# Kernel tuning notes

Hardware: AMD Instinct MI355X
Metric: run time of the kernel (lower is better)

Reference implementation:

```python
import jax, jax.numpy as jnp
import numpy as np

B, R, Z, H = 2048, 512, 256, 512
T = 16           # num_steps
NL = 3           # num_layers
SCALE = 0.05     # param init scale


def setup_inputs() -> dict:
    key = jax.random.key(0)
    ks = jax.random.split(key, 8)
    return {
        "r": jax.random.normal(ks[0], (B, R), jnp.float32),
        "noise0": jax.random.normal(ks[1], (B, Z), jnp.float32),
        "noise": jax.random.normal(ks[2], (T, B, Z), jnp.float32),
        "W0": jax.random.normal(ks[3], (Z + R, H), jnp.float32) * SCALE,
        "b0": jnp.zeros((H,), jnp.float32),
        "Wh": jax.random.normal(ks[4], (H, H), jnp.float32) * SCALE,
        "bh": jnp.zeros((H,), jnp.float32),
        "Wo": jax.random.normal(ks[5], (H, Z), jnp.float32) * SCALE,
        "bo": jnp.zeros((Z,), jnp.float32),
        "Wt": jax.random.normal(ks[6], (1, Z + R), jnp.float32) * SCALE,
        "bt": jnp.zeros((Z + R,), jnp.float32),
    }


def reference(r, noise0, noise, W0, b0, Wh, bh, Wo, bo, Wt, bt):
    dt = jnp.float32(1.0 / T)
    sqrt_dt = jnp.sqrt(dt)

    def score_fn(z, t_scaled):
        # time_embedding: Linear(1, z+r) then non-linearity, added to [z, r]
        temb = jax.nn.relu(t_scaled * Wt[0] + bt)            # (Z+R,)
        h = jnp.concatenate([z, r], axis=-1) + temb          # (B, Z+R)
        h = h @ W0 + b0                                      # (B, H)
        # faithful to buggy nn.Sequential: act x (NL-1), then the SAME
        # shared Linear(h,h) applied (NL-1) times
        for _ in range(NL - 1):
            h = jax.nn.relu(h)
        for _ in range(NL - 1):
            h = h @ Wh + bh
        return h @ Wo + bo                                   # (B, Z)

    def step(z_prev, xs):
        t, eps = xs
        # Euler-Maruyama forward step: mu = z + score * dt, sigma = sqrt(dt)
        z_mu = z_prev + score_fn(z_prev, t * dt) * dt
        z_sigma = sqrt_dt * jnp.ones_like(z_mu)
        z = z_mu + z_sigma * eps                             # reparameterize
        return z, (z, z_mu, z_sigma)

    ts = jnp.arange(1, T + 1, dtype=jnp.float32)
    # z_0 ~ N(0, get_sigma(0)=1)
    z0 = noise0
    _, (zs, mus, sigmas) = jax.lax.scan(step, z0, (ts, noise))
    zs = jnp.concatenate([z0[None], zs], axis=0)             # (T+1, B, Z)
    mus = jnp.concatenate([jnp.zeros((1, B, Z), zs.dtype), mus], axis=0)
    sigmas = jnp.concatenate([jnp.ones((1, B, Z), zs.dtype), sigmas], axis=0)
    return jnp.stack([zs, mus, sigmas])                      # (3, T+1, B, Z)
```

## Files before the change

kernel.cpp:

```cpp
#include <hip/hip_runtime.h>


typedef __bf16 bf16_t;
typedef bf16_t bf16x8 __attribute__((ext_vector_type(8)));
typedef float f32x4 __attribute__((ext_vector_type(4)));

#define MFMA16(a, b, c) __builtin_amdgcn_mfma_f32_16x16x32_bf16((a), (b), (c), 0, 0, 0)

__device__ __forceinline__ void glds16(const void* gsrc, void* ldst) {
  __builtin_amdgcn_global_load_lds(
      (const __attribute__((address_space(1))) unsigned int*)gsrc,
      (__attribute__((address_space(3))) unsigned int*)ldst, 16, 0, 0);
}

__device__ __forceinline__ void pack_body(const float* __restrict__ src, bf16_t* __restrict__ dst,
                                          int K, int N, int tid0) {
  int NT = N >> 4;
  if (tid0 >= (K >> 5) * NT * 64) return;
  int l = tid0 & 63, grp = tid0 >> 6;
  int nt = grp % NT, kt = grp / NT;
  int rr = l & 15, gg = l >> 4;
  const float* s = src + (size_t)(kt * 32 + 8 * gg) * N + nt * 16 + rr;
  bf16_t* d = dst + (size_t)tid0 * 8;
#pragma unroll
  for (int j = 0; j < 8; ++j) d[j] = (bf16_t)s[(size_t)j * N];
}

__global__ __launch_bounds__(256) void p1_kernel(
    const float* __restrict__ r, const float* __restrict__ noise0,
    const float* __restrict__ W0, const float* __restrict__ Wh,
    const float* __restrict__ Wo, const float* __restrict__ Wt, const float* __restrict__ bt,
    bf16_t* __restrict__ r_bf, bf16_t* __restrict__ Wh_bf,
    bf16_t* __restrict__ W0zp, bf16_t* __restrict__ W0rp, bf16_t* __restrict__ Wop,
    float* __restrict__ tadd, float* __restrict__ out)
{
  const int SLAB = 2048 * 256;
  const int SZ = 17 * SLAB;
  int bid = blockIdx.x, tid = threadIdx.x;
  if (bid < 9728) {
    int i = (bid * 256 + tid) * 4;
    if (i >= 19 * SLAB) return;
    float4 v; int dst;
    if (i < 17 * SLAB) { float x = (i < SLAB) ? 1.0f : 0.25f; v = make_float4(x, x, x, x); dst = 2 * SZ + i; }
    else if (i < 18 * SLAB) { v = make_float4(0.f, 0.f, 0.f, 0.f); dst = SZ + (i - 17 * SLAB); }
    else { v = *(const float4*)(noise0 + (i - 18 * SLAB)); dst = i - 18 * SLAB; }
    *(float4*)(out + dst) = v;
  } else if (bid < 10752) {
    int i = ((bid - 9728) * 256 + tid) * 4;
#pragma unroll
    for (int j = 0; j < 4; ++j) r_bf[i + j] = (bf16_t)r[i + j];
  } else if (bid < 11008) {
    int i = ((bid - 10752) * 256 + tid) * 4;
#pragma unroll
    for (int j = 0; j < 4; ++j) Wh_bf[i + j] = (bf16_t)Wh[i + j];
  } else if (bid < 11072) {
    pack_body(W0, W0zp, 256, 512, (bid - 11008) * 256 + tid);
  } else if (bid < 11200) {
    pack_body(W0 + 256 * 512, W0rp, 512, 512, (bid - 11072) * 256 + tid);
  } else if (bid < 11264) {
    pack_body(Wo, Wop, 512, 256, (bid - 11200) * 256 + tid);
  } else {
    int rel = bid - 11264;
    int t = rel >> 1, n = (rel & 1) * 256 + tid;
    float ts = (t + 1) * 0.0625f;
    float s = 0.f;
#pragma unroll 4
    for (int k = 0; k < 768; ++k) {
      float e = fmaxf(ts * Wt[k] + bt[k], 0.f);
      s = fmaf(e, W0[(size_t)k * 512 + n], s);
    }
    tadd[t * 512 + n] = s;
  }
}

__device__ __forceinline__ void gemm_dev(
    const bf16_t* __restrict__ A, const bf16_t* __restrict__ Bp, const float* __restrict__ bias,
    float* __restrict__ C, bf16_t* __restrict__ Cp,
    int N, int K, int rt, int ct, bool useBias, bool writeRM, bool writePacked)
{
  int tid = threadIdx.x;
  int l = tid & 63, w = tid >> 6;
  int rr = l & 15, gg = l >> 4;
  int rowbase = rt * 64 + w * 16, colbase = ct * 64;
  int NT = N >> 4;
  const bf16x8* Bv = (const bf16x8*)Bp;
  f32x4 acc[4] = {};
  for (int kt = 0; kt < (K >> 5); ++kt) {
    bf16x8 af = *(const bf16x8*)(A + (size_t)(rowbase + rr) * K + kt * 32 + 8 * gg);
#pragma unroll
    for (int nt = 0; nt < 4; ++nt) {
      bf16x8 bf = Bv[(size_t)(kt * NT + (colbase >> 4) + nt) * 64 + l];
      acc[nt] = MFMA16(af, bf, acc[nt]);
    }
  }
#pragma unroll
  for (int nt = 0; nt < 4; ++nt) {
    int col = colbase + nt * 16 + rr;
    float bv = useBias ? bias[col] : 0.f;
#pragma unroll
    for (int q = 0; q < 4; ++q) {
      int row = rowbase + 4 * gg + q;
      float vv = acc[nt][q] + bv;
      if (writeRM) C[(size_t)row * N + col] = vv;
      if (writePacked) {
        int ktr = row >> 5;
        int lane2 = (2 * (w & 1) + (gg >> 1)) * 16 + rr;
        int jj = 4 * (gg & 1) + q;
        Cp[(size_t)((ktr * NT + (colbase >> 4) + nt) * 64 + lane2) * 8 + jj] = (bf16_t)vv;
      }
    }
  }
}

__global__ __launch_bounds__(256) void p2_kernel(
    const bf16_t* __restrict__ r_bf, const bf16_t* __restrict__ W0rp, const float* __restrict__ b0,
    float* __restrict__ baseb,
    const bf16_t* __restrict__ Wh_bf, const bf16_t* __restrict__ Wop,
    float* __restrict__ T3f, bf16_t* __restrict__ T3p)
{
  int bid = blockIdx.x;
  if (bid < 256) gemm_dev(r_bf, W0rp, b0, baseb, nullptr, 512, 512, bid & 31, bid >> 5, true, true, false);
  else           gemm_dev(Wh_bf, Wop, nullptr, T3f, T3p, 256, 512, (bid - 256) & 7, (bid - 256) >> 3, false, true, true);
}

__global__ __launch_bounds__(256) void p3_kernel(
    const bf16_t* __restrict__ Wh_bf, const bf16_t* __restrict__ T3p, bf16_t* __restrict__ Wfp,
    const float* __restrict__ bh, const float* __restrict__ T3f, const float* __restrict__ Wo,
    const float* __restrict__ bo, float* __restrict__ bo2)
{
  int bid = blockIdx.x;
  if (bid < 32) {
    gemm_dev(Wh_bf, T3p, nullptr, nullptr, Wfp, 256, 512, bid & 7, bid >> 3, false, false, true);
  } else {
    int n = threadIdx.x;
    float s = bo[n];
#pragma unroll 4
    for (int k = 0; k < 512; ++k)
      s = fmaf(bh[k], T3f[k * 256 + n] + Wo[k * 256 + n], s);
    bo2[n] = s;
  }
}

__global__ __launch_bounds__(512) void diffusion_main_kernel(
    const bf16_t* __restrict__ wpack,
    const float* __restrict__ base,
    const float* __restrict__ tadd,
    const float* __restrict__ bo2,
    const float* __restrict__ noise0,
    const float* __restrict__ noise,
    float* __restrict__ out)
{
  __shared__ bf16_t zbuf[16 * 256];
  __shared__ bf16_t abuf[16 * 512];
  __shared__ char wbuf[2][65536];
  const int tid = threadIdx.x;
  const int w = tid >> 6, l = tid & 63;
  const int rr = l & 15, gg = l >> 4;
  const int brow = blockIdx.x << 4;
  const char* wdata = (const char*)wpack;

  f32x4 base_reg[4];
#pragma unroll
  for (int nt = 0; nt < 4; ++nt)
#pragma unroll
    for (int q = 0; q < 4; ++q)
      base_reg[nt][q] = base[(size_t)(brow + 4 * gg + q) * 512 + w * 64 + nt * 16 + rr];
  float bo_reg[2];
#pragma unroll
  for (int nt = 0; nt < 2; ++nt) bo_reg[nt] = bo2[w * 32 + nt * 16 + rr];

  f32x4 zst[2];
#pragma unroll
  for (int nt = 0; nt < 2; ++nt)
#pragma unroll
    for (int q = 0; q < 4; ++q)
      zst[nt][q] = noise0[(size_t)(brow + 4 * gg + q) * 256 + w * 32 + nt * 16 + rr];
#pragma unroll
  for (int nt = 0; nt < 2; ++nt)
#pragma unroll
    for (int q = 0; q < 4; ++q) {
      int row = 4 * gg + q, col = w * 32 + nt * 16 + rr;
      zbuf[(row * 256 + col) ^ ((row & 7) << 3)] = (bf16_t)zst[nt][q];
    }

  {
    const char* src = wdata;
    char* dstl = &wbuf[0][0];
#pragma unroll
    for (int it = 0; it < 8; ++it)
      glds16(src + it * 8192 + w * 1024 + l * 16, dstl + it * 8192 + w * 1024);
  }

  f32x4 acc1[4];
  f32x4 acc2[2];
  bf16x8 zf[8];
  float ep[2][4];
  float tv[4];

#pragma unroll 1
  for (int cc = 0; cc < 128; ++cc) {
    __syncthreads();
    if (cc + 1 < 128) {
      const char* src = wdata + (size_t)((cc + 1) & 7) * 65536;
      char* dstl = &wbuf[(cc + 1) & 1][0];
#pragma unroll
      for (int it = 0; it < 8; ++it)
        glds16(src + it * 8192 + w * 1024 + l * 16, dstl + it * 8192 + w * 1024);
    }
    const char* wb = &wbuf[cc & 1][0];
    const int ph = cc & 7;
    const int t = cc >> 3;

    if (ph < 4) {
      if (ph == 0) {
#pragma unroll
        for (int nt = 0; nt < 2; ++nt)
#pragma unroll
          for (int q = 0; q < 4; ++q)
            ep[nt][q] = noise[((size_t)t * 2048 + brow + 4 * gg + q) * 256 + w * 32 + nt * 16 + rr];
#pragma unroll
        for (int nt = 0; nt < 4; ++nt) tv[nt] = tadd[t * 512 + w * 64 + nt * 16 + rr];
#pragma unroll
        for (int kt = 0; kt < 8; ++kt) {
          int e = (rr * 256 + kt * 32 + 8 * gg) ^ ((rr & 7) << 3);
          zf[kt] = *(const bf16x8*)&zbuf[e];
        }
#pragma unroll
        for (int nt = 0; nt < 4; ++nt)
#pragma unroll
          for (int q = 0; q < 4; ++q) acc1[nt][q] = base_reg[nt][q] + tv[nt];
      }
#pragma unroll
      for (int ktl = 0; ktl < 2; ++ktl) {
        int fbase = ktl * 32 + w * 4;
#pragma unroll
        for (int nt = 0; nt < 4; ++nt) {
          bf16x8 wfrag = *(const bf16x8*)(wb + ((size_t)(fbase + nt) * 64 + l) * 16);
          acc1[nt] = MFMA16(zf[2 * ph + ktl], wfrag, acc1[nt]);
        }
      }
      if (ph == 3) {
#pragma unroll
        for (int nt = 0; nt < 4; ++nt)
#pragma unroll
          for (int q = 0; q < 4; ++q) {
            int row = 4 * gg + q, col = w * 64 + nt * 16 + rr;
            abuf[(row * 512 + col) ^ ((row & 7) << 3)] = (bf16_t)fmaxf(acc1[nt][q], 0.f);
          }
      }
    } else {
      if (ph == 4) {
#pragma unroll
        for (int nt = 0; nt < 2; ++nt)
#pragma unroll
          for (int q = 0; q < 4; ++q) acc2[nt][q] = bo_reg[nt];
      }
      const int pc = ph - 4;
#pragma unroll
      for (int ktl = 0; ktl < 4; ++ktl) {
        int ktg = pc * 4 + ktl;
        int e = (rr * 512 + ktg * 32 + 8 * gg) ^ ((rr & 7) << 3);
        bf16x8 afr = *(const bf16x8*)&abuf[e];
        int fbase = ktl * 16 + w * 2;
#pragma unroll
        for (int nt = 0; nt < 2; ++nt) {
          bf16x8 wfrag = *(const bf16x8*)(wb + ((size_t)(fbase + nt) * 64 + l) * 16);
          acc2[nt] = MFMA16(afr, wfrag, acc2[nt]);
        }
      }
      if (ph == 7) {
#pragma unroll
        for (int nt = 0; nt < 2; ++nt)
#pragma unroll
          for (int q = 0; q < 4; ++q) {
            int row = 4 * gg + q, col = w * 32 + nt * 16 + rr;
            int grow = brow + row;
            float mu = fmaf(acc2[nt][q], 0.0625f, zst[nt][q]);
            float zn = fmaf(ep[nt][q], 0.25f, mu);
            zst[nt][q] = zn;
            out[((size_t)(t + 1) * 2048 + grow) * 256 + col] = zn;
            out[((size_t)(17 + t + 1) * 2048 + grow) * 256 + col] = mu;
            zbuf[(row * 256 + col) ^ ((row & 7) << 3)] = (bf16_t)zn;
          }
      }
    }
  }
}

extern "C" void kernel_launch(void* const* d_in, const int* in_sizes, int n_in,
                              void* d_out, int out_size, void* d_ws, size_t ws_size,
                              hipStream_t stream) {
  const float* r   = (const float*)d_in[0];
  const float* n0  = (const float*)d_in[1];
  const float* nz  = (const float*)d_in[2];
  const float* W0  = (const float*)d_in[3];
  const float* b0  = (const float*)d_in[4];
  const float* Wh  = (const float*)d_in[5];
  const float* bh  = (const float*)d_in[6];
  const float* Wo  = (const float*)d_in[7];
  const float* bo  = (const float*)d_in[8];
  const float* Wt  = (const float*)d_in[9];
  const float* bt  = (const float*)d_in[10];
  float* out = (float*)d_out;

  char* ws = (char*)d_ws;
  size_t off = 0;
  auto alloc = [&](size_t bytes) -> char* {
    char* p = ws + off;
    off += (bytes + 255) & ~(size_t)255;
    return p;
  };
  bf16_t* r_bf  = (bf16_t*)alloc((size_t)2048 * 512 * 2);
  bf16_t* Wh_bf = (bf16_t*)alloc((size_t)512 * 512 * 2);
  bf16_t* wpack = (bf16_t*)alloc((size_t)512 * 1024);
  bf16_t* W0zp  = wpack;
  bf16_t* Wfp   = wpack + 131072;
  bf16_t* W0rp  = (bf16_t*)alloc((size_t)512 * 512 * 2);
  bf16_t* Wop   = (bf16_t*)alloc((size_t)512 * 256 * 2);
  float*  T3f   = (float*) alloc((size_t)512 * 256 * 4);
  bf16_t* T3p   = (bf16_t*)alloc((size_t)512 * 256 * 2);
  float*  baseb = (float*) alloc((size_t)2048 * 512 * 4);
  float*  taddb = (float*) alloc((size_t)16 * 512 * 4);
  float*  bo2b  = (float*) alloc((size_t)256 * 4);
  if (off > ws_size) return;

  p1_kernel<<<11296, 256, 0, stream>>>(r, n0, W0, Wh, Wo, Wt, bt,
                                       r_bf, Wh_bf, W0zp, W0rp, Wop, taddb, out);
  p2_kernel<<<288, 256, 0, stream>>>(r_bf, W0rp, b0, baseb, Wh_bf, Wop, T3f, T3p);
  p3_kernel<<<33, 256, 0, stream>>>(Wh_bf, T3p, Wfp, bh, T3f, Wo, bo, bo2b);
  diffusion_main_kernel<<<128, 512, 0, stream>>>(wpack, baseb, taddb, bo2b, n0, nz, out);
}
```

Baseline: 423.1 us.

## Keep fused weight in registers and stream W0z fragments directly from global

Drops the double-buffered 128KB LDS weight staging fed by global_load_lds. The fused Wh·Wo weight slice for each wave now sits permanently in registers (32 bf16x8 fragments), and W0z fragments are loaded straight from global/L2 on every timestep. The loop runs once per timestep with two barriers instead of 128 chunk iterations with a barrier each. This removes LDS traffic and per-chunk synchronisation, but raises register pressure (launch_bounds 512,2) and puts global load latency on the path of the first GEMM.

Result: slower. 475.9 us (+12.5%).

```diff
diff --git a/kernel.cpp b/kernel.cpp
--- a/kernel.cpp
+++ b/kernel.cpp
@@ -6,12 +6,6 @@
 typedef float f32x4 __attribute__((ext_vector_type(4)));
 
 #define MFMA16(a, b, c) __builtin_amdgcn_mfma_f32_16x16x32_bf16((a), (b), (c), 0, 0, 0)
-
-__device__ __forceinline__ void glds16(const void* gsrc, void* ldst) {
-  __builtin_amdgcn_global_load_lds(
-      (const __attribute__((address_space(1))) unsigned int*)gsrc,
-      (__attribute__((address_space(3))) unsigned int*)ldst, 16, 0, 0);
-}
 
 __device__ __forceinline__ void pack_body(const float* __restrict__ src, bf16_t* __restrict__ dst,
                                           int K, int N, int tid0) {
@@ -141,8 +135,9 @@
   }
 }
 
-__global__ __launch_bounds__(512) void diffusion_main_kernel(
-    const bf16_t* __restrict__ wpack,
+__global__ __launch_bounds__(512, 2) void diffusion_main_kernel(
+    const bf16_t* __restrict__ W0zp,
+    const bf16_t* __restrict__ Wfp,
     const float* __restrict__ base,
     const float* __restrict__ tadd,
     const float* __restrict__ bo2,
@@ -152,12 +147,22 @@
 {
   __shared__ bf16_t zbuf[16 * 256];
   __shared__ bf16_t abuf[16 * 512];
-  __shared__ char wbuf[2][65536];
   const int tid = threadIdx.x;
   const int w = tid >> 6, l = tid & 63;
   const int rr = l & 15, gg = l >> 4;
   const int brow = blockIdx.x << 4;
-  const char* wdata = (const char*)wpack;
+  const size_t SLAB = 2048 * 256;
+  const size_t SZ = 17 * SLAB;
+
+  const bf16x8* W0v = (const bf16x8*)W0zp;
+  const bf16x8* Wfv = (const bf16x8*)Wfp;
+
+  bf16x8 wfres[16][2];
+#pragma unroll
+  for (int kt = 0; kt < 16; ++kt)
+#pragma unroll
+    for (int nt = 0; nt < 2; ++nt)
+      wfres[kt][nt] = Wfv[(size_t)(kt * 16 + w * 2 + nt) * 64 + l];
 
   f32x4 base_reg[4];
 #pragma unroll
@@ -182,108 +187,83 @@
       int row = 4 * gg + q, col = w * 32 + nt * 16 + rr;
       zbuf[(row * 256 + col) ^ ((row & 7) << 3)] = (bf16_t)zst[nt][q];
     }
-
-  {
-    const char* src = wdata;
-    char* dstl = &wbuf[0][0];
-#pragma unroll
-    for (int it = 0; it < 8; ++it)
-      glds16(src + it * 8192 + w * 1024 + l * 16, dstl + it * 8192 + w * 1024);
-  }
-
-  f32x4 acc1[4];
-  f32x4 acc2[2];
-  bf16x8 zf[8];
-  float ep[2][4];
-  float tv[4];
+  __syncthreads();
 
 #pragma unroll 1
-  for (int cc = 0; cc < 128; ++cc) {
+  for (int t = 0; t < 16; ++t) {
+    float ep[2][4];
+#pragma unroll
+    for (int nt = 0; nt < 2; ++nt)
+#pragma unroll
+      for (int q = 0; q < 4; ++q)
+        ep[nt][q] = noise[((size_t)t * 2048 + brow + 4 * gg + q) * 256 + w * 32 + nt * 16 + rr];
+
+    f32x4 acc1[4];
+#pragma unroll
+    for (int nt = 0; nt < 4; ++nt) {
+      float tv = tadd[t * 512 + w * 64 + nt * 16 + rr];
+#pragma unroll
+      for (int q = 0; q < 4; ++q) acc1[nt][q] = base_reg[nt][q] + tv;
+    }
+
+#pragma unroll
+    for (int c = 0; c < 4; ++c) {
+      bf16x8 wst[2][4];
+#pragma unroll
+      for (int ktl = 0; ktl < 2; ++ktl)
+#pragma unroll
+        for (int nt = 0; nt < 4; ++nt)
+          wst[ktl][nt] = W0v[(size_t)((2 * c + ktl) * 32 + w * 4 + nt) * 64 + l];
+      bf16x8 zc[2];
+#pragma unroll
+      for (int ktl = 0; ktl < 2; ++ktl) {
+        int e = (rr * 256 + (2 * c + ktl) * 32 + 8 * gg) ^ ((rr & 7) << 3);
+        zc[ktl] = *(const bf16x8*)&zbuf[e];
+      }
+#pragma unroll
+      for (int ktl = 0; ktl < 2; ++ktl)
+#pragma unroll
+        for (int nt = 0; nt < 4; ++nt)
+          acc1[nt] = MFMA16(zc[ktl], wst[ktl][nt], acc1[nt]);
+    }
+
+#pragma unroll
+    for (int nt = 0; nt < 4; ++nt)
+#pragma unroll
+      for (int q = 0; q < 4; ++q) {
+        int row = 4 * gg + q, col = w * 64 + nt * 16 + rr;
+        abuf[(row * 512 + col) ^ ((row & 7) << 3)] = (bf16_t)fmaxf(acc1[nt][q], 0.f);
+      }
     __syncthreads();
-    if (cc + 1 < 128) {
-      const char* src = wdata + (size_t)((cc + 1) & 7) * 65536;
-      char* dstl = &wbuf[(cc + 1) & 1][0];
-#pragma unroll
-      for (int it = 0; it < 8; ++it)
-        glds16(src + it * 8192 + w * 1024 + l * 16, dstl + it * 8192 + w * 1024);
-    }
-    const char* wb = &wbuf[cc & 1][0];
-    const int ph = cc & 7;
-    const int t = cc >> 3;
-
-    if (ph < 4) {
-      if (ph == 0) {
-#pragma unroll
-        for (int nt = 0; nt < 2; ++nt)
-#pragma unroll
-          for (int q = 0; q < 4; ++q)
-            ep[nt][q] = noise[((size_t)t * 2048 + brow + 4 * gg + q) * 256 + w * 32 + nt * 16 + rr];
-#pragma unroll
-        for (int nt = 0; nt < 4; ++nt) tv[nt] = tadd[t * 512 + w * 64 + nt * 16 + rr];
-#pragma unroll
-        for (int kt = 0; kt < 8; ++kt) {
-          int e = (rr * 256 + kt * 32 + 8 * gg) ^ ((rr & 7) << 3);
-          zf[kt] = *(const bf16x8*)&zbuf[e];
-        }
-#pragma unroll
-        for (int nt = 0; nt < 4; ++nt)
-#pragma unroll
-          for (int q = 0; q < 4; ++q) acc1[nt][q] = base_reg[nt][q] + tv[nt];
+
+    f32x4 acc2[2];
+#pragma unroll
+    for (int nt = 0; nt < 2; ++nt)
+#pragma unroll
+      for (int q = 0; q < 4; ++q) acc2[nt][q] = bo_reg[nt];
+#pragma unroll
+    for (int kt = 0; kt < 16; ++kt) {
+      int e = (rr * 512 + kt * 32 + 8 * gg) ^ ((rr & 7) << 3);
+      bf16x8 af = *(const bf16x8*)&abuf[e];
+#pragma unroll
+      for (int nt = 0; nt < 2; ++nt)
+        acc2[nt] = MFMA16(af, wfres[kt][nt], acc2[nt]);
+    }
+
+#pragma unroll
+    for (int nt = 0; nt < 2; ++nt)
+#pragma unroll
+      for (int q = 0; q < 4; ++q) {
+        int row = 4 * gg + q, col = w * 32 + nt * 16 + rr;
+        int grow = brow + row;
+        float mu = fmaf(acc2[nt][q], 0.0625f, zst[nt][q]);
+        float zn = fmaf(ep[nt][q], 0.25f, mu);
+        zst[nt][q] = zn;
+        out[((size_t)(t + 1) * 2048 + grow) * 256 + col] = zn;
+        out[SZ + ((size_t)(t + 1) * 2048 + grow) * 256 + col] = mu;
+        zbuf[(row * 256 + col) ^ ((row & 7) << 3)] = (bf16_t)zn;
       }
-#pragma unroll
-      for (int ktl = 0; ktl < 2; ++ktl) {
-        int fbase = ktl * 32 + w * 4;
-#pragma unroll
-        for (int nt = 0; nt < 4; ++nt) {
-          bf16x8 wfrag = *(const bf16x8*)(wb + ((size_t)(fbase + nt) * 64 + l) * 16);
-          acc1[nt] = MFMA16(zf[2 * ph + ktl], wfrag, acc1[nt]);
-        }
-      }
-      if (ph == 3) {
-#pragma unroll
-        for (int nt = 0; nt < 4; ++nt)
-#pragma unroll
-          for (int q = 0; q < 4; ++q) {
-            int row = 4 * gg + q, col = w * 64 + nt * 16 + rr;
-            abuf[(row * 512 + col) ^ ((row & 7) << 3)] = (bf16_t)fmaxf(acc1[nt][q], 0.f);
-          }
-      }
-    } else {
-      if (ph == 4) {
-#pragma unroll
-        for (int nt = 0; nt < 2; ++nt)
-#pragma unroll
-          for (int q = 0; q < 4; ++q) acc2[nt][q] = bo_reg[nt];
-      }
-      const int pc = ph - 4;
-#pragma unroll
-      for (int ktl = 0; ktl < 4; ++ktl) {
-        int ktg = pc * 4 + ktl;
-        int e = (rr * 512 + ktg * 32 + 8 * gg) ^ ((rr & 7) << 3);
-        bf16x8 afr = *(const bf16x8*)&abuf[e];
-        int fbase = ktl * 16 + w * 2;
-#pragma unroll
-        for (int nt = 0; nt < 2; ++nt) {
-          bf16x8 wfrag = *(const bf16x8*)(wb + ((size_t)(fbase + nt) * 64 + l) * 16);
-          acc2[nt] = MFMA16(afr, wfrag, acc2[nt]);
-        }
-      }
-      if (ph == 7) {
-#pragma unroll
-        for (int nt = 0; nt < 2; ++nt)
-#pragma unroll
-          for (int q = 0; q < 4; ++q) {
-            int row = 4 * gg + q, col = w * 32 + nt * 16 + rr;
-            int grow = brow + row;
-            float mu = fmaf(acc2[nt][q], 0.0625f, zst[nt][q]);
-            float zn = fmaf(ep[nt][q], 0.25f, mu);
-            zst[nt][q] = zn;
-            out[((size_t)(t + 1) * 2048 + grow) * 256 + col] = zn;
-            out[((size_t)(17 + t + 1) * 2048 + grow) * 256 + col] = mu;
-            zbuf[(row * 256 + col) ^ ((row & 7) << 3)] = (bf16_t)zn;
-          }
-      }
-    }
+    __syncthreads();
   }
 }
 
@@ -312,9 +292,8 @@
   };
   bf16_t* r_bf  = (bf16_t*)alloc((size_t)2048 * 512 * 2);
   bf16_t* Wh_bf = (bf16_t*)alloc((size_t)512 * 512 * 2);
-  bf16_t* wpack = (bf16_t*)alloc((size_t)512 * 1024);
-  bf16_t* W0zp  = wpack;
-  bf16_t* Wfp   = wpack + 131072;
+  bf16_t* W0zp  = (bf16_t*)alloc((size_t)256 * 512 * 2);
+  bf16_t* Wfp   = (bf16_t*)alloc((size_t)512 * 256 * 2);
   bf16_t* W0rp  = (bf16_t*)alloc((size_t)512 * 512 * 2);
   bf16_t* Wop   = (bf16_t*)alloc((size_t)512 * 256 * 2);
   float*  T3f   = (float*) alloc((size_t)512 * 256 * 4);
@@ -328,5 +307,5 @@
                                        r_bf, Wh_bf, W0zp, W0rp, Wop, taddb, out);
   p2_kernel<<<288, 256, 0, stream>>>(r_bf, W0rp, b0, baseb, Wh_bf, Wop, T3f, T3p);
   p3_kernel<<<33, 256, 0, stream>>>(Wh_bf, T3p, Wfp, bh, T3f, Wo, bo, bo2b);
-  diffusion_main_kernel<<<128, 512, 0, stream>>>(wpack, baseb, taddb, bo2b, n0, nz, out);
-}
+  diffusion_main_kernel<<<128, 512, 0, stream>>>(W0zp, Wfp, baseb, taddb, bo2b, n0, nz, out);
+}
```
